# Kernel tuning notes

Hardware: AMD Instinct MI355X
Metric: run time of the kernel (lower is better)

Reference implementation:

```python
import jax, jax.numpy as jnp
from jax import lax
import numpy as np

B, CIN, H, W = 1, 3, 96, 96
Q = 65536
C = 64
CU = C * 9              # feat_unfold channels
IN_DIM = CU + 2 + 2     # q_feat + rel_coord + rel_cell
HID = 256
OUT = 3
EPS_SHIFT = 1e-6


def setup_inputs():
    key = jax.random.key(0)
    ks = jax.random.split(key, 16)
    inp = jax.random.normal(ks[0], (B, CIN, H, W), jnp.float32)
    coord = jax.random.uniform(ks[1], (B, Q, 2), jnp.float32, -1.0, 1.0)
    cell = jnp.full((B, Q, 2), 2.0 / 256.0, jnp.float32)  # cell size of a 256x256 output grid
    enc_w = jax.random.normal(ks[2], (C, CIN, 3, 3), jnp.float32) * 0.1
    enc_b = jnp.zeros((C,), jnp.float32)
    dims = [IN_DIM, HID, HID, HID, HID, OUT]
    out = {"inp": inp, "coord": coord, "cell": cell, "enc_w": enc_w, "enc_b": enc_b}
    for i in range(5):
        out[f"w{i}"] = jax.random.normal(ks[3 + i], (dims[i], dims[i + 1]), jnp.float32) * (1.0 / np.sqrt(dims[i]))
        out[f"b{i}"] = jnp.zeros((dims[i + 1],), jnp.float32)
    return out


def _unfold3x3(feat):
    # F.unfold(feat, 3, padding=1).reshape(b, c*9, h, w): channel order c-major, kernel row-major
    b, c, h, w = feat.shape
    p = jnp.pad(feat, ((0, 0), (0, 0), (1, 1), (1, 1)))
    pats = jnp.stack([p[:, :, ki:ki + h, kj:kj + w] for ki in range(3) for kj in range(3)], axis=2)
    return pats.reshape(b, c * 9, h, w)


def _nearest_idx(c, n):
    # torch grid_sample nearest, align_corners=False: unnormalize then round-half-even (nearbyint)
    ix = (c + 1.0) * n / 2.0 - 0.5
    return jnp.clip(jnp.round(ix), 0, n - 1).astype(jnp.int32)


def _gather(fmap, iy, ix):
    # fmap [B,C,H,W], iy/ix [B,Q] -> [B,Q,C]
    return jax.vmap(lambda f, y, x: f[:, y, x].T)(fmap, iy, ix)


def _mlp(x, ws, bs):
    for wgt, b in zip(ws[:-1], bs[:-1]):
        x = jax.nn.relu(x @ wgt + b)
    return x @ ws[-1] + bs[-1]


def reference(inp, coord, cell, enc_w, enc_b, w0, b0, w1, b1, w2, b2, w3, b3, w4, b4):
    ws = [w0, w1, w2, w3, w4]
    bs = [b0, b1, b2, b3, b4]
    # encoder: 3x3 conv, SAME padding
    feat = lax.conv_general_dilated(inp, enc_w, (1, 1), 'SAME') + enc_b[None, :, None, None]
    feat = _unfold3x3(feat)                     # [B, C*9, H, W]
    h, w = feat.shape[2], feat.shape[3]
    rx, ry = 1.0 / h, 1.0 / w                   # 2/r/2
    # make_coord pixel centers
    fcy = -1.0 + (2.0 * jnp.arange(h, dtype=jnp.float32) + 1.0) / h   # [H]
    fcx = -1.0 + (2.0 * jnp.arange(w, dtype=jnp.float32) + 1.0) / w   # [W]
    bnd = 1.0 - 1e-6
    rel_cell = cell * jnp.array([h, w], dtype=cell.dtype)             # [B,Q,2]

    preds, areas = [], []
    for vx in (-1.0, 1.0):
        for vy in (-1.0, 1.0):
            c0 = jnp.clip(coord[..., 0] + vx * rx + EPS_SHIFT, -bnd, bnd)
            c1 = jnp.clip(coord[..., 1] + vy * ry + EPS_SHIFT, -bnd, bnd)
            iy = _nearest_idx(c0, h)            # coord[...,0] indexes dim H
            ix = _nearest_idx(c1, w)
            q_feat = _gather(feat, iy, ix)      # [B,Q,CU]
            rel0 = (coord[..., 0] - fcy[iy]) * h
            rel1 = (coord[..., 1] - fcx[ix]) * w
            mlp_in = jnp.concatenate([q_feat, rel0[..., None], rel1[..., None], rel_cell], axis=-1)
            pred = _mlp(mlp_in.reshape(-1, IN_DIM), ws, bs).reshape(coord.shape[0], coord.shape[1], OUT)
            preds.append(pred)
            areas.append(jnp.abs(rel0 * rel1) + 1e-9)

    tot_area = areas[0] + areas[1] + areas[2] + areas[3]
    # local-ensemble diagonal swap
    areas = [areas[3], areas[2], areas[1], areas[0]]
    ret = 0.0
    for pred, area in zip(preds, areas):
        ret = ret + pred * (area / tot_area)[..., None]
    return ret
```

## Files before the change

kernel.cpp:

```cpp
#include <hip/hip_runtime.h>
#include <math.h>

#define NPOS 9216

using half8  = __attribute__((ext_vector_type(8))) _Float16;
using f32x4  = __attribute__((ext_vector_type(4))) float;
using f32x16 = __attribute__((ext_vector_type(16))) float;

#define OFF_FEATT 0u
#define OFF_A0    1229312u
#define OFF_WF32  5947904u
#define OFF_WF4   6341120u
#define OFF_WB    6349312u

#define NB_FEAT 2401
#define NB_PA   768
#define NB_PW4  16
#define NB_PB   576

#define BAR() do { asm volatile("s_waitcnt lgkmcnt(0)" ::: "memory"); \
                   __builtin_amdgcn_s_barrier();                      \
                   asm volatile("" ::: "memory"); } while (0)

__global__ __launch_bounds__(256) void setup_kernel(
    const float* __restrict__ inp, const float* __restrict__ enc_w,
    const float* __restrict__ enc_b, const float* __restrict__ w0,
    const float* __restrict__ w1, const float* __restrict__ w2,
    const float* __restrict__ w3, const float* __restrict__ w4,
    _Float16* __restrict__ featT, _Float16* __restrict__ wf32,
    _Float16* __restrict__ wf4, _Float16* __restrict__ wB)
{
    int blk = blockIdx.x;
    const int t = threadIdx.x;

    if (blk < NB_FEAT) {
        int pp = blk * 4 + (t >> 6);
        int c  = t & 63;
        int py = pp / 98, px = pp - py * 98;
        float acc = 0.0f;
        if (py >= 1 && py <= 96 && px >= 1 && px <= 96) {
            int y = py - 1, x = px - 1;
            acc = enc_b[c];
            #pragma unroll
            for (int cin = 0; cin < 3; ++cin) {
                #pragma unroll
                for (int ky = 0; ky < 3; ++ky) {
                    int yy = y + ky - 1;
                    if (yy < 0 || yy >= 96) continue;
                    #pragma unroll
                    for (int kx = 0; kx < 3; ++kx) {
                        int xx = x + kx - 1;
                        if (xx < 0 || xx >= 96) continue;
                        acc = fmaf(inp[cin * NPOS + yy * 96 + xx],
                                   enc_w[c * 27 + cin * 9 + ky * 3 + kx], acc);
                    }
                }
            }
        }
        featT[pp * 64 + c] = (_Float16)acc;
        return;
    }
    blk -= NB_FEAT;
    if (blk < NB_PA) {
        int idx = blk * 256 + t;
        int l = idx >> 16;
        int r = idx & 65535;
        int j    = r & 7;
        int lane = (r >> 3) & 63;
        int nt32 = (r >> 9) & 7;
        int ks   = r >> 12;
        int n = nt32 * 32 + (lane & 31);
        int k = ks * 16 + ((lane >> 5) << 3) + j;
        const float* W = (l == 0) ? w1 : (l == 1) ? w2 : w3;
        wf32[idx] = (_Float16)W[k * 256 + n];
        return;
    }
    blk -= NB_PA;
    if (blk < NB_PW4) {
        int idx = blk * 256 + t;
        int j    = idx & 7;
        int lane = (idx >> 3) & 63;
        int ks   = idx >> 9;
        int n = lane & 15;
        int k = ks * 32 + ((lane >> 4) << 3) + j;
        wf4[idx] = (n < 3) ? (_Float16)w4[k * 3 + n] : (_Float16)0.0f;
        return;
    }
    blk -= NB_PW4;
    {
        int idx = blk * 256 + t;
        int j    = idx & 7;
        int lane = (idx >> 3) & 63;
        int ntB  = (idx >> 9) & 15;
        int ks   = (idx >> 13) & 1;
        int t9   = idx >> 14;
        int c = ks * 32 + ((lane >> 4) << 3) + j;
        int n = ntB * 16 + (lane & 15);
        wB[idx] = (_Float16)w0[(c * 9 + t9) * 256 + n];
    }
}

__global__ __launch_bounds__(256) void a0_mfma(const _Float16* __restrict__ featT,
                                               const _Float16* __restrict__ wB,
                                               const float* __restrict__ b0,
                                               _Float16* __restrict__ A0)
{
    const int lane = threadIdx.x & 63;
    const int tile = blockIdx.x * 4 + (threadIdx.x >> 6);
    const int l15  = lane & 15;
    const int l4   = lane >> 4;
    int r = tile * 16 + l15;
    int y = r / 96, x = r - y * 96;

    f32x4 acc[16];
    #pragma unroll
    for (int nt = 0; nt < 16; ++nt) acc[nt] = (f32x4){0.f, 0.f, 0.f, 0.f};

    #pragma unroll
    for (int t9 = 0; t9 < 9; ++t9) {
        int ki = t9 / 3, kj = t9 - ki * 3;
        const _Float16* ap = featT + ((y + ki) * 98 + (x + kj)) * 64 + l4 * 8;
        #pragma unroll
        for (int ks = 0; ks < 2; ++ks) {
            half8 a = *(const half8*)(ap + ks * 32);
            const _Float16* bp = wB + ((t9 * 2 + ks) * 16 * 64 + lane) * 8;
            #pragma unroll
            for (int nt = 0; nt < 16; ++nt) {
                half8 b = *(const half8*)(bp + nt * 512);
                acc[nt] = __builtin_amdgcn_mfma_f32_16x16x32_f16(a, b, acc[nt], 0, 0, 0);
            }
        }
    }
    int rb = tile * 16 + l4 * 4;
    #pragma unroll
    for (int nt = 0; nt < 16; ++nt) {
        float bb = b0[nt * 16 + l15];
        #pragma unroll
        for (int i = 0; i < 4; ++i)
            A0[(rb + i) * 256 + nt * 16 + l15] = (_Float16)(acc[nt][i] + bb);
    }
}

__device__ __forceinline__ void hidden_layer32(
    _Float16 (*h)[264], const _Float16* __restrict__ W,
    const float* __restrict__ bias, const _Float16* __restrict__ Wpre,
    bool preIsFinal,
    half8 p0, half8 p1, half8 p2, half8 p3,
    half8& q0, half8& q1, half8& q2, half8& q3,
    int wn, int lane)
{
    const int l31 = lane & 31;
    const int l5  = lane >> 5;
    f32x16 a00 = {}, a01 = {}, a10 = {}, a11 = {};

    {
        half8 Av0 = *(const half8*)&h[l31][l5 * 8];
        half8 Av1 = *(const half8*)&h[32 + l31][l5 * 8];
        a00 = __builtin_amdgcn_mfma_f32_32x32x16_f16(Av0, p0, a00, 0, 0, 0);
        a01 = __builtin_amdgcn_mfma_f32_32x32x16_f16(Av0, p1, a01, 0, 0, 0);
        a10 = __builtin_amdgcn_mfma_f32_32x32x16_f16(Av1, p0, a10, 0, 0, 0);
        a11 = __builtin_amdgcn_mfma_f32_32x32x16_f16(Av1, p1, a11, 0, 0, 0);
        Av0 = *(const half8*)&h[l31][16 + l5 * 8];
        Av1 = *(const half8*)&h[32 + l31][16 + l5 * 8];
        a00 = __builtin_amdgcn_mfma_f32_32x32x16_f16(Av0, p2, a00, 0, 0, 0);
        a01 = __builtin_amdgcn_mfma_f32_32x32x16_f16(Av0, p3, a01, 0, 0, 0);
        a10 = __builtin_amdgcn_mfma_f32_32x32x16_f16(Av1, p2, a10, 0, 0, 0);
        a11 = __builtin_amdgcn_mfma_f32_32x32x16_f16(Av1, p3, a11, 0, 0, 0);
    }
    #pragma unroll
    for (int ks = 2; ks < 16; ++ks) {
        half8 Av0 = *(const half8*)&h[l31][ks * 16 + l5 * 8];
        half8 Av1 = *(const half8*)&h[32 + l31][ks * 16 + l5 * 8];
        const _Float16* bp = W + (ks * 8 + wn * 2) * 512 + lane * 8;
        half8 Bv0 = *(const half8*)bp;
        half8 Bv1 = *(const half8*)(bp + 512);
        a00 = __builtin_amdgcn_mfma_f32_32x32x16_f16(Av0, Bv0, a00, 0, 0, 0);
        a01 = __builtin_amdgcn_mfma_f32_32x32x16_f16(Av0, Bv1, a01, 0, 0, 0);
        a10 = __builtin_amdgcn_mfma_f32_32x32x16_f16(Av1, Bv0, a10, 0, 0, 0);
        a11 = __builtin_amdgcn_mfma_f32_32x32x16_f16(Av1, Bv1, a11, 0, 0, 0);
    }

    if (preIsFinal) {
        q0 = *(const half8*)&Wpre[(0 * 64 + lane) * 8];
        q1 = *(const half8*)&Wpre[(1 * 64 + lane) * 8];
        q2 = *(const half8*)&Wpre[(2 * 64 + lane) * 8];
        q3 = *(const half8*)&Wpre[(3 * 64 + lane) * 8];
    } else {
        const _Float16* bp0 = Wpre + (wn * 2) * 512 + lane * 8;
        const _Float16* bp1 = Wpre + (8 + wn * 2) * 512 + lane * 8;
        q0 = *(const half8*)bp0;
        q1 = *(const half8*)(bp0 + 512);
        q2 = *(const half8*)bp1;
        q3 = *(const half8*)(bp1 + 512);
    }

    BAR();
    float bv0 = bias[wn * 64 + l31];
    float bv1 = bias[wn * 64 + 32 + l31];
    #pragma unroll
    for (int reg = 0; reg < 16; ++reg) {
        int rr = (reg & 3) + ((reg >> 2) << 3) + (l5 << 2);
        int c0 = wn * 64 + l31;
        h[rr][c0]           = (_Float16)fmaxf(a00[reg] + bv0, 0.0f);
        h[rr][c0 + 32]      = (_Float16)fmaxf(a01[reg] + bv1, 0.0f);
        h[rr + 32][c0]      = (_Float16)fmaxf(a10[reg] + bv0, 0.0f);
        h[rr + 32][c0 + 32] = (_Float16)fmaxf(a11[reg] + bv1, 0.0f);
    }
    BAR();
}

__global__ __launch_bounds__(256, 4) void fused_kernel(
    const _Float16* __restrict__ A0, const float* __restrict__ coord,
    const float* __restrict__ cell, const float* __restrict__ w0,
    const float* __restrict__ b1, const float* __restrict__ b2,
    const float* __restrict__ b3, const float* __restrict__ b4,
    const _Float16* __restrict__ wf32, const _Float16* __restrict__ wf4,
    float* __restrict__ out)
{
    __shared__ _Float16 h[64][264];
    __shared__ float pred[64][4];
    __shared__ float s_rel0[64], s_rel1[64], s_rc0[64], s_rc1[64], s_area[64];
    __shared__ int   s_pos[64];

    const int t   = threadIdx.x;
    const int blk = blockIdx.x;

    if (t < 64) {
        int r = blk * 64 + t;
        int q = r >> 2;
        int j = r & 3;
        float vx = (j & 2) ? 1.0f : -1.0f;
        float vy = (j & 1) ? 1.0f : -1.0f;
        float c0 = coord[q * 2 + 0];
        float c1 = coord[q * 2 + 1];
        const float rr  = 1.0f / 96.0f;
        const float bnd = 1.0f - 1e-6f;
        float sc0 = fminf(fmaxf(fmaf(vx, rr, c0) + 1e-6f, -bnd), bnd);
        float sc1 = fminf(fmaxf(fmaf(vy, rr, c1) + 1e-6f, -bnd), bnd);
        float fy = (sc0 + 1.0f) * 48.0f - 0.5f;
        float fx = (sc1 + 1.0f) * 48.0f - 0.5f;
        int iy = (int)rintf(fy); iy = iy < 0 ? 0 : (iy > 95 ? 95 : iy);
        int ix = (int)rintf(fx); ix = ix < 0 ? 0 : (ix > 95 ? 95 : ix);
        float fcy = -1.0f + (2.0f * (float)iy + 1.0f) / 96.0f;
        float fcx = -1.0f + (2.0f * (float)ix + 1.0f) / 96.0f;
        float rel0 = (c0 - fcy) * 96.0f;
        float rel1 = (c1 - fcx) * 96.0f;
        s_pos[t]  = iy * 96 + ix;
        s_rel0[t] = rel0;
        s_rel1[t] = rel1;
        s_rc0[t]  = cell[q * 2 + 0] * 96.0f;
        s_rc1[t]  = cell[q * 2 + 1] * 96.0f;
        s_area[t] = fabsf(rel0 * rel1) + 1e-9f;
    }
    __syncthreads();

    {
        const int cg = t & 31;
        const int rg = t >> 5;
        const float* wbase = w0 + 576 * 256 + cg * 8;
        float4 wa0 = *(const float4*)(wbase);
        float4 wa1 = *(const float4*)(wbase + 4);
        float4 wb0 = *(const float4*)(wbase + 256);
        float4 wb1 = *(const float4*)(wbase + 260);
        float4 wc0 = *(const float4*)(wbase + 512);
        float4 wc1 = *(const float4*)(wbase + 516);
        float4 wd0 = *(const float4*)(wbase + 768);
        float4 wd1 = *(const float4*)(wbase + 772);
        #pragma unroll
        for (int rr = 0; rr < 8; ++rr) {
            const int m = rg * 8 + rr;
            half8 qv = *(const half8*)&A0[s_pos[m] * 256 + cg * 8];
            float r0 = s_rel0[m], r1 = s_rel1[m], rc0 = s_rc0[m], rc1 = s_rc1[m];
            half8 o;
            float v;
            v = (float)qv[0]; v = fmaf(r0,wa0.x,v); v = fmaf(r1,wb0.x,v); v = fmaf(rc0,wc0.x,v); v = fmaf(rc1,wd0.x,v); o[0] = (_Float16)fmaxf(v,0.f);
            v = (float)qv[1]; v = fmaf(r0,wa0.y,v); v = fmaf(r1,wb0.y,v); v = fmaf(rc0,wc0.y,v); v = fmaf(rc1,wd0.y,v); o[1] = (_Float16)fmaxf(v,0.f);
            v = (float)qv[2]; v = fmaf(r0,wa0.z,v); v = fmaf(r1,wb0.z,v); v = fmaf(rc0,wc0.z,v); v = fmaf(rc1,wd0.z,v); o[2] = (_Float16)fmaxf(v,0.f);
            v = (float)qv[3]; v = fmaf(r0,wa0.w,v); v = fmaf(r1,wb0.w,v); v = fmaf(rc0,wc0.w,v); v = fmaf(rc1,wd0.w,v); o[3] = (_Float16)fmaxf(v,0.f);
            v = (float)qv[4]; v = fmaf(r0,wa1.x,v); v = fmaf(r1,wb1.x,v); v = fmaf(rc0,wc1.x,v); v = fmaf(rc1,wd1.x,v); o[4] = (_Float16)fmaxf(v,0.f);
            v = (float)qv[5]; v = fmaf(r0,wa1.y,v); v = fmaf(r1,wb1.y,v); v = fmaf(rc0,wc1.y,v); v = fmaf(rc1,wd1.y,v); o[5] = (_Float16)fmaxf(v,0.f);
            v = (float)qv[6]; v = fmaf(r0,wa1.z,v); v = fmaf(r1,wb1.z,v); v = fmaf(rc0,wc1.z,v); v = fmaf(rc1,wd1.z,v); o[6] = (_Float16)fmaxf(v,0.f);
            v = (float)qv[7]; v = fmaf(r0,wa1.w,v); v = fmaf(r1,wb1.w,v); v = fmaf(rc0,wc1.w,v); v = fmaf(rc1,wd1.w,v); o[7] = (_Float16)fmaxf(v,0.f);
            *(half8*)&h[m][cg * 8] = o;
        }
    }

    const int wave = t >> 6;
    const int lane = t & 63;
    const int wn   = wave;

    half8 p0, p1, p2, p3, q0, q1, q2, q3;
    {
        const _Float16* bp0 = wf32 + (wn * 2) * 512 + lane * 8;
        const _Float16* bp1 = wf32 + (8 + wn * 2) * 512 + lane * 8;
        p0 = *(const half8*)bp0;
        p1 = *(const half8*)(bp0 + 512);
        p2 = *(const half8*)bp1;
        p3 = *(const half8*)(bp1 + 512);
    }
    BAR();

    hidden_layer32(h, wf32,             b1, wf32 + 65536,     false, p0,p1,p2,p3, q0,q1,q2,q3, wn, lane);
    hidden_layer32(h, wf32 + 65536,     b2, wf32 + 2 * 65536, false, q0,q1,q2,q3, p0,p1,p2,p3, wn, lane);
    hidden_layer32(h, wf32 + 2 * 65536, b3, wf4,              true,  p0,p1,p2,p3, q0,q1,q2,q3, wn, lane);

    {
        const int l15 = lane & 15;
        const int l4  = lane >> 4;
        f32x4 acc = (f32x4){0.f, 0.f, 0.f, 0.f};
        half8 a;
        a = *(const half8*)&h[wave * 16 + l15][0 * 32 + l4 * 8];
        acc = __builtin_amdgcn_mfma_f32_16x16x32_f16(a, q0, acc, 0, 0, 0);
        a = *(const half8*)&h[wave * 16 + l15][1 * 32 + l4 * 8];
        acc = __builtin_amdgcn_mfma_f32_16x16x32_f16(a, q1, acc, 0, 0, 0);
        a = *(const half8*)&h[wave * 16 + l15][2 * 32 + l4 * 8];
        acc = __builtin_amdgcn_mfma_f32_16x16x32_f16(a, q2, acc, 0, 0, 0);
        a = *(const half8*)&h[wave * 16 + l15][3 * 32 + l4 * 8];
        acc = __builtin_amdgcn_mfma_f32_16x16x32_f16(a, q3, acc, 0, 0, 0);
        #pragma unroll
        for (int ks = 4; ks < 8; ++ks) {
            a = *(const half8*)&h[wave * 16 + l15][ks * 32 + l4 * 8];
            half8 b = *(const half8*)&wf4[(ks * 64 + lane) * 8];
            acc = __builtin_amdgcn_mfma_f32_16x16x32_f16(a, b, acc, 0, 0, 0);
        }
        if (l15 < 3) {
            float bv = b4[l15];
            #pragma unroll
            for (int i = 0; i < 4; ++i)
                pred[wave * 16 + l4 * 4 + i][l15] = acc[i] + bv;
        }
    }
    BAR();

    if (t < 48) {
        int ql = t / 3;
        int o  = t - ql * 3;
        int mb = ql * 4;
        float a0 = s_area[mb + 0];
        float a1 = s_area[mb + 1];
        float a2 = s_area[mb + 2];
        float a3 = s_area[mb + 3];
        float tot = a0 + a1 + a2 + a3;
        float rv = pred[mb + 0][o] * a3 + pred[mb + 1][o] * a2 +
                   pred[mb + 2][o] * a1 + pred[mb + 3][o] * a0;
        out[(blk * 16 + ql) * 3 + o] = rv / tot;
    }
}

extern "C" void kernel_launch(void* const* d_in, const int* in_sizes, int n_in,
                              void* d_out, int out_size, void* d_ws, size_t ws_size,
                              hipStream_t stream)
{
    (void)in_sizes; (void)n_in; (void)out_size; (void)ws_size;
    const float* inp   = (const float*)d_in[0];
    const float* coord = (const float*)d_in[1];
    const float* cell  = (const float*)d_in[2];
    const float* enc_w = (const float*)d_in[3];
    const float* enc_b = (const float*)d_in[4];
    const float* w0 = (const float*)d_in[5];
    const float* b0 = (const float*)d_in[6];
    const float* w1 = (const float*)d_in[7];
    const float* b1 = (const float*)d_in[8];
    const float* w2 = (const float*)d_in[9];
    const float* b2 = (const float*)d_in[10];
    const float* w3 = (const float*)d_in[11];
    const float* b3 = (const float*)d_in[12];
    const float* w4 = (const float*)d_in[13];
    const float* b4 = (const float*)d_in[14];
    float* outp = (float*)d_out;

    char* ws = (char*)d_ws;
    _Float16* featT = (_Float16*)(ws + OFF_FEATT);
    _Float16* A0    = (_Float16*)(ws + OFF_A0);
    _Float16* wf32  = (_Float16*)(ws + OFF_WF32);
    _Float16* wf4   = (_Float16*)(ws + OFF_WF4);
    _Float16* wB    = (_Float16*)(ws + OFF_WB);

    setup_kernel<<<dim3(NB_FEAT + NB_PA + NB_PW4 + NB_PB), dim3(256), 0, stream>>>(
        inp, enc_w, enc_b, w0, w1, w2, w3, w4, featT, wf32, wf4, wB);
    a0_mfma<<<dim3(144), dim3(256), 0, stream>>>(featT, wB, b0, A0);
    fused_kernel<<<dim3(4096), dim3(256), 0, stream>>>(A0, coord, cell, w0,
                                                       b1, b2, b3, b4, wf32, wf4, outp);
}
```

Baseline: 291.9 us.

## Enlarge fused MLP tile to 256 rows with 8 waves and 3-deep weight prefetch

The fused MLP kernel now processes 256 rows per block with 512 threads, arranged as a 2x4 wave grid. Each wave computes a 128x64 output tile, so every B-fragment loaded from global memory feeds 4 row tiles instead of 2. Weight fragments are prefetched three k-steps ahead in a rotating register buffer, and the next layer's first fragments are loaded during the tail. The cost is a larger LDS footprint (~135KB per block), more accumulator registers, and fewer resident blocks, which may reduce latency hiding.

```diff
diff --git a/kernel.cpp b/kernel.cpp
--- a/kernel.cpp
+++ b/kernel.cpp
@@ -141,75 +141,88 @@
     }
 }
 
-__device__ __forceinline__ void hidden_layer32(
-    _Float16 (*h)[264], const _Float16* __restrict__ W,
-    const float* __restrict__ bias, const _Float16* __restrict__ Wpre,
-    bool preIsFinal,
-    half8 p0, half8 p1, half8 p2, half8 p3,
-    half8& q0, half8& q1, half8& q2, half8& q3,
-    int wn, int lane)
+__device__ __forceinline__ void hidden_layer_big(
+    _Float16 (*h)[264],
+    const _Float16* __restrict__ W, const float* __restrict__ bias,
+    const _Float16* __restrict__ Wnext, const _Float16* __restrict__ wf4,
+    bool nextIsFinal,
+    half8 p0, half8 p1, half8 p2, half8 p3, half8 p4, half8 p5,
+    half8& q0, half8& q1, half8& q2, half8& q3, half8& q4, half8& q5,
+    int wm, int wn, int lane)
 {
     const int l31 = lane & 31;
     const int l5  = lane >> 5;
-    f32x16 a00 = {}, a01 = {}, a10 = {}, a11 = {};
-
-    {
-        half8 Av0 = *(const half8*)&h[l31][l5 * 8];
-        half8 Av1 = *(const half8*)&h[32 + l31][l5 * 8];
-        a00 = __builtin_amdgcn_mfma_f32_32x32x16_f16(Av0, p0, a00, 0, 0, 0);
-        a01 = __builtin_amdgcn_mfma_f32_32x32x16_f16(Av0, p1, a01, 0, 0, 0);
-        a10 = __builtin_amdgcn_mfma_f32_32x32x16_f16(Av1, p0, a10, 0, 0, 0);
-        a11 = __builtin_amdgcn_mfma_f32_32x32x16_f16(Av1, p1, a11, 0, 0, 0);
-        Av0 = *(const half8*)&h[l31][16 + l5 * 8];
-        Av1 = *(const half8*)&h[32 + l31][16 + l5 * 8];
-        a00 = __builtin_amdgcn_mfma_f32_32x32x16_f16(Av0, p2, a00, 0, 0, 0);
-        a01 = __builtin_amdgcn_mfma_f32_32x32x16_f16(Av0, p3, a01, 0, 0, 0);
-        a10 = __builtin_amdgcn_mfma_f32_32x32x16_f16(Av1, p2, a10, 0, 0, 0);
-        a11 = __builtin_amdgcn_mfma_f32_32x32x16_f16(Av1, p3, a11, 0, 0, 0);
-    }
-    #pragma unroll
-    for (int ks = 2; ks < 16; ++ks) {
-        half8 Av0 = *(const half8*)&h[l31][ks * 16 + l5 * 8];
-        half8 Av1 = *(const half8*)&h[32 + l31][ks * 16 + l5 * 8];
-        const _Float16* bp = W + (ks * 8 + wn * 2) * 512 + lane * 8;
-        half8 Bv0 = *(const half8*)bp;
-        half8 Bv1 = *(const half8*)(bp + 512);
-        a00 = __builtin_amdgcn_mfma_f32_32x32x16_f16(Av0, Bv0, a00, 0, 0, 0);
-        a01 = __builtin_amdgcn_mfma_f32_32x32x16_f16(Av0, Bv1, a01, 0, 0, 0);
-        a10 = __builtin_amdgcn_mfma_f32_32x32x16_f16(Av1, Bv0, a10, 0, 0, 0);
-        a11 = __builtin_amdgcn_mfma_f32_32x32x16_f16(Av1, Bv1, a11, 0, 0, 0);
-    }
-
-    if (preIsFinal) {
-        q0 = *(const half8*)&Wpre[(0 * 64 + lane) * 8];
-        q1 = *(const half8*)&Wpre[(1 * 64 + lane) * 8];
-        q2 = *(const half8*)&Wpre[(2 * 64 + lane) * 8];
-        q3 = *(const half8*)&Wpre[(3 * 64 + lane) * 8];
-    } else {
-        const _Float16* bp0 = Wpre + (wn * 2) * 512 + lane * 8;
-        const _Float16* bp1 = Wpre + (8 + wn * 2) * 512 + lane * 8;
-        q0 = *(const half8*)bp0;
-        q1 = *(const half8*)(bp0 + 512);
-        q2 = *(const half8*)bp1;
-        q3 = *(const half8*)(bp1 + 512);
+    const int ra  = wm * 128 + l31;
+    const _Float16* bbase = W + (wn * 2) * 512 + lane * 8;
+
+    f32x16 acc[4][2];
+    #pragma unroll
+    for (int rt = 0; rt < 4; ++rt)
+        #pragma unroll
+        for (int ct = 0; ct < 2; ++ct)
+            acc[rt][ct] = (f32x16){};
+
+    half8 B[3][2];
+    B[0][0] = p0; B[0][1] = p1;
+    B[1][0] = p2; B[1][1] = p3;
+    B[2][0] = p4; B[2][1] = p5;
+
+    #pragma unroll
+    for (int ks = 0; ks < 16; ++ks) {
+        const int cs = ks % 3;
+        half8 bu0 = B[cs][0];
+        half8 bu1 = B[cs][1];
+        if (ks <= 12) {
+            B[cs][0] = *(const half8*)(bbase + (ks + 3) * 4096);
+            B[cs][1] = *(const half8*)(bbase + (ks + 3) * 4096 + 512);
+        } else {
+            const int nk = ks - 13;
+            if (nextIsFinal) {
+                half8 f0 = *(const half8*)&wf4[((2 * nk + 0) * 64 + lane) * 8];
+                half8 f1 = *(const half8*)&wf4[((2 * nk + 1) * 64 + lane) * 8];
+                if (nk == 0) { q0 = f0; q1 = f1; }
+                else if (nk == 1) { q2 = f0; q3 = f1; }
+                else { q4 = f0; q5 = f1; }
+            } else {
+                const _Float16* nb = Wnext + (nk * 8 + wn * 2) * 512 + lane * 8;
+                half8 f0 = *(const half8*)nb;
+                half8 f1 = *(const half8*)(nb + 512);
+                if (nk == 0) { q0 = f0; q1 = f1; }
+                else if (nk == 1) { q2 = f0; q3 = f1; }
+                else { q4 = f0; q5 = f1; }
+            }
+        }
+        half8 a0 = *(const half8*)&h[ra +  0][ks * 16 + l5 * 8];
+        half8 a1 = *(const half8*)&h[ra + 32][ks * 16 + l5 * 8];
+        half8 a2 = *(const half8*)&h[ra + 64][ks * 16 + l5 * 8];
+        half8 a3 = *(const half8*)&h[ra + 96][ks * 16 + l5 * 8];
+        acc[0][0] = __builtin_amdgcn_mfma_f32_32x32x16_f16(a0, bu0, acc[0][0], 0, 0, 0);
+        acc[0][1] = __builtin_amdgcn_mfma_f32_32x32x16_f16(a0, bu1, acc[0][1], 0, 0, 0);
+        acc[1][0] = __builtin_amdgcn_mfma_f32_32x32x16_f16(a1, bu0, acc[1][0], 0, 0, 0);
+        acc[1][1] = __builtin_amdgcn_mfma_f32_32x32x16_f16(a1, bu1, acc[1][1], 0, 0, 0);
+        acc[2][0] = __builtin_amdgcn_mfma_f32_32x32x16_f16(a2, bu0, acc[2][0], 0, 0, 0);
+        acc[2][1] = __builtin_amdgcn_mfma_f32_32x32x16_f16(a2, bu1, acc[2][1], 0, 0, 0);
+        acc[3][0] = __builtin_amdgcn_mfma_f32_32x32x16_f16(a3, bu0, acc[3][0], 0, 0, 0);
+        acc[3][1] = __builtin_amdgcn_mfma_f32_32x32x16_f16(a3, bu1, acc[3][1], 0, 0, 0);
     }
 
     BAR();
     float bv0 = bias[wn * 64 + l31];
     float bv1 = bias[wn * 64 + 32 + l31];
     #pragma unroll
-    for (int reg = 0; reg < 16; ++reg) {
-        int rr = (reg & 3) + ((reg >> 2) << 3) + (l5 << 2);
-        int c0 = wn * 64 + l31;
-        h[rr][c0]           = (_Float16)fmaxf(a00[reg] + bv0, 0.0f);
-        h[rr][c0 + 32]      = (_Float16)fmaxf(a01[reg] + bv1, 0.0f);
-        h[rr + 32][c0]      = (_Float16)fmaxf(a10[reg] + bv0, 0.0f);
-        h[rr + 32][c0 + 32] = (_Float16)fmaxf(a11[reg] + bv1, 0.0f);
+    for (int rt = 0; rt < 4; ++rt) {
+        #pragma unroll
+        for (int reg = 0; reg < 16; ++reg) {
+            int rr = wm * 128 + rt * 32 + (reg & 3) + ((reg >> 2) << 3) + (l5 << 2);
+            int c0 = wn * 64 + l31;
+            h[rr][c0]      = (_Float16)fmaxf(acc[rt][0][reg] + bv0, 0.0f);
+            h[rr][c0 + 32] = (_Float16)fmaxf(acc[rt][1][reg] + bv1, 0.0f);
+        }
     }
     BAR();
 }
 
-__global__ __launch_bounds__(256, 4) void fused_kernel(
+__global__ __launch_bounds__(512, 2) void fused_kernel(
     const _Float16* __restrict__ A0, const float* __restrict__ coord,
     const float* __restrict__ cell, const float* __restrict__ w0,
     const float* __restrict__ b1, const float* __restrict__ b2,
@@ -217,16 +230,31 @@
     const _Float16* __restrict__ wf32, const _Float16* __restrict__ wf4,
     float* __restrict__ out)
 {
-    __shared__ _Float16 h[64][264];
-    __shared__ float pred[64][4];
-    __shared__ float s_rel0[64], s_rel1[64], s_rc0[64], s_rc1[64], s_area[64];
-    __shared__ int   s_pos[64];
-
-    const int t   = threadIdx.x;
-    const int blk = blockIdx.x;
-
-    if (t < 64) {
-        int r = blk * 64 + t;
+    __shared__ _Float16 h[256][264];
+    __shared__ float pred[256][4];
+    __shared__ float s_rel0[256], s_rel1[256], s_rc0[256], s_rc1[256], s_area[256];
+    __shared__ int   s_pos[256];
+
+    const int t    = threadIdx.x;
+    const int blk  = blockIdx.x;
+    const int wave = t >> 6;
+    const int lane = t & 63;
+    const int wm   = wave & 1;
+    const int wn   = wave >> 1;
+
+    half8 p0, p1, p2, p3, p4, p5, q0, q1, q2, q3, q4, q5;
+    {
+        const _Float16* bp = wf32 + (wn * 2) * 512 + lane * 8;
+        p0 = *(const half8*)(bp);
+        p1 = *(const half8*)(bp + 512);
+        p2 = *(const half8*)(bp + 4096);
+        p3 = *(const half8*)(bp + 4096 + 512);
+        p4 = *(const half8*)(bp + 8192);
+        p5 = *(const half8*)(bp + 8192 + 512);
+    }
+
+    if (t < 256) {
+        int r = blk * 256 + t;
         int q = r >> 2;
         int j = r & 3;
         float vx = (j & 2) ? 1.0f : -1.0f;
@@ -267,8 +295,8 @@
         float4 wd0 = *(const float4*)(wbase + 768);
         float4 wd1 = *(const float4*)(wbase + 772);
         #pragma unroll
-        for (int rr = 0; rr < 8; ++rr) {
-            const int m = rg * 8 + rr;
+        for (int rr = 0; rr < 16; ++rr) {
+            const int m = rg * 16 + rr;
             half8 qv = *(const half8*)&A0[s_pos[m] * 256 + cg * 8];
             float r0 = s_rel0[m], r1 = s_rel1[m], rc0 = s_rc0[m], rc1 = s_rc1[m];
             half8 o;
@@ -284,55 +312,40 @@
             *(half8*)&h[m][cg * 8] = o;
         }
     }
-
-    const int wave = t >> 6;
-    const int lane = t & 63;
-    const int wn   = wave;
-
-    half8 p0, p1, p2, p3, q0, q1, q2, q3;
-    {
-        const _Float16* bp0 = wf32 + (wn * 2) * 512 + lane * 8;
-        const _Float16* bp1 = wf32 + (8 + wn * 2) * 512 + lane * 8;
-        p0 = *(const half8*)bp0;
-        p1 = *(const half8*)(bp0 + 512);
-        p2 = *(const half8*)bp1;
-        p3 = *(const half8*)(bp1 + 512);
-    }
     BAR();
 
-    hidden_layer32(h, wf32,             b1, wf32 + 65536,     false, p0,p1,p2,p3, q0,q1,q2,q3, wn, lane);
-    hidden_layer32(h, wf32 + 65536,     b2, wf32 + 2 * 65536, false, q0,q1,q2,q3, p0,p1,p2,p3, wn, lane);
-    hidden_layer32(h, wf32 + 2 * 65536, b3, wf4,              true,  p0,p1,p2,p3, q0,q1,q2,q3, wn, lane);
+    hidden_layer_big(h, wf32,             b1, wf32 + 65536,     wf4, false, p0,p1,p2,p3,p4,p5, q0,q1,q2,q3,q4,q5, wm, wn, lane);
+    hidden_layer_big(h, wf32 + 65536,     b2, wf32 + 2 * 65536, wf4, false, q0,q1,q2,q3,q4,q5, p0,p1,p2,p3,p4,p5, wm, wn, lane);
+    hidden_layer_big(h, wf32 + 2 * 65536, b3, (const _Float16*)0, wf4, true, p0,p1,p2,p3,p4,p5, q0,q1,q2,q3,q4,q5, wm, wn, lane);
 
     {
         const int l15 = lane & 15;
         const int l4  = lane >> 4;
-        f32x4 acc = (f32x4){0.f, 0.f, 0.f, 0.f};
-        half8 a;
-        a = *(const half8*)&h[wave * 16 + l15][0 * 32 + l4 * 8];
-        acc = __builtin_amdgcn_mfma_f32_16x16x32_f16(a, q0, acc, 0, 0, 0);
-        a = *(const half8*)&h[wave * 16 + l15][1 * 32 + l4 * 8];
-        acc = __builtin_amdgcn_mfma_f32_16x16x32_f16(a, q1, acc, 0, 0, 0);
-        a = *(const half8*)&h[wave * 16 + l15][2 * 32 + l4 * 8];
-        acc = __builtin_amdgcn_mfma_f32_16x16x32_f16(a, q2, acc, 0, 0, 0);
-        a = *(const half8*)&h[wave * 16 + l15][3 * 32 + l4 * 8];
-        acc = __builtin_amdgcn_mfma_f32_16x16x32_f16(a, q3, acc, 0, 0, 0);
-        #pragma unroll
-        for (int ks = 4; ks < 8; ++ks) {
-            a = *(const half8*)&h[wave * 16 + l15][ks * 32 + l4 * 8];
-            half8 b = *(const half8*)&wf4[(ks * 64 + lane) * 8];
-            acc = __builtin_amdgcn_mfma_f32_16x16x32_f16(a, b, acc, 0, 0, 0);
+        const int rowb = wave * 32;
+        f32x4 acc0 = (f32x4){0.f, 0.f, 0.f, 0.f};
+        f32x4 acc1 = (f32x4){0.f, 0.f, 0.f, 0.f};
+        half8 b6 = *(const half8*)&wf4[(6 * 64 + lane) * 8];
+        half8 b7 = *(const half8*)&wf4[(7 * 64 + lane) * 8];
+        half8 bf[8] = {q0, q1, q2, q3, q4, q5, b6, b7};
+        #pragma unroll
+        for (int ks = 0; ks < 8; ++ks) {
+            half8 a0 = *(const half8*)&h[rowb + l15][ks * 32 + l4 * 8];
+            half8 a1 = *(const half8*)&h[rowb + 16 + l15][ks * 32 + l4 * 8];
+            acc0 = __builtin_amdgcn_mfma_f32_16x16x32_f16(a0, bf[ks], acc0, 0, 0, 0);
+            acc1 = __builtin_amdgcn_mfma_f32_16x16x32_f16(a1, bf[ks], acc1, 0, 0, 0);
         }
         if (l15 < 3) {
             float bv = b4[l15];
             #pragma unroll
-            for (int i = 0; i < 4; ++i)
-                pred[wave * 16 + l4 * 4 + i][l15] = acc[i] + bv;
+            for (int i = 0; i < 4; ++i) {
+                pred[rowb + l4 * 4 + i][l15]      = acc0[i] + bv;
+                pred[rowb + 16 + l4 * 4 + i][l15] = acc1[i] + bv;
+            }
         }
     }
     BAR();
 
-    if (t < 48) {
+    if (t < 192) {
         int ql = t / 3;
         int o  = t - ql * 3;
         int mb = ql * 4;
@@ -343,7 +356,7 @@
         float tot = a0 + a1 + a2 + a3;
         float rv = pred[mb + 0][o] * a3 + pred[mb + 1][o] * a2 +
                    pred[mb + 2][o] * a1 + pred[mb + 3][o] * a0;
-        out[(blk * 16 + ql) * 3 + o] = rv / tot;
+        out[(blk * 64 + ql) * 3 + o] = rv / tot;
     }
 }
 
@@ -379,6 +392,6 @@
     setup_kernel<<<dim3(NB_FEAT + NB_PA + NB_PW4 + NB_PB), dim3(256), 0, stream>>>(
         inp, enc_w, enc_b, w0, w1, w2, w3, w4, featT, wf32, wf4, wB);
     a0_mfma<<<dim3(144), dim3(256), 0, stream>>>(featT, wB, b0, A0);
-    fused_kernel<<<dim3(4096), dim3(256), 0, stream>>>(A0, coord, cell, w0,
+    fused_kernel<<<dim3(1024), dim3(512), 0, stream>>>(A0, coord, cell, w0,
                                                        b1, b2, b3, b4, wf32, wf4, outp);
 }
```

Result: no change. 287.6 us (-1.5%).
